# Kernel tuning notes

Hardware: AMD Instinct MI355X
Metric: run time of the kernel (lower is better)

The kernel has to match this reference:

```python
import jax, jax.numpy as jnp
import numpy as np

B, L, D, H = 4, 1024, 1024, 16
HD = D // H  # 64
MAX_LEN = 1024


def setup_inputs() -> dict:
    key = jax.random.key(0)
    k1, k2, k3, k4 = jax.random.split(key, 4)
    x = jax.random.normal(k1, (B, L, D), dtype=jnp.float32)
    W_qkv = jax.random.normal(k2, (D, 3 * D), dtype=jnp.float32) * (1.0 / np.sqrt(D))
    W_proj = jax.random.normal(k3, (D, D), dtype=jnp.float32) * (1.0 / np.sqrt(D))
    b_proj = jnp.zeros((D,), dtype=jnp.float32)
    rel_pos_emb = jax.random.normal(k4, (2 * MAX_LEN - 1, HD), dtype=jnp.float32)
    return {"x": x, "W_qkv": W_qkv, "W_proj": W_proj, "b_proj": b_proj,
            "rel_pos_emb": rel_pos_emb}


def reference(x, W_qkv, W_proj, b_proj, rel_pos_emb):
    b, l, d = x.shape
    scale = 1.0 / np.sqrt(HD)
    # fused qkv projection: [B, L, 3, H, HD]
    qkv = (x @ W_qkv).reshape(b, l, 3, H, HD)
    q = jnp.transpose(qkv[:, :, 0], (0, 2, 1, 3))  # [B, H, L, HD]
    k = jnp.transpose(qkv[:, :, 1], (0, 2, 1, 3))
    v = jnp.transpose(qkv[:, :, 2], (0, 2, 1, 3))
    # content scores
    attn = jnp.einsum('bhld,bhmd->bhlm', q, k) * scale
    # relative position scores: pos_indices[i, j] = (j - i) + (L - 1)
    pos_indices = (jnp.arange(l)[None, :] - jnp.arange(l)[:, None]) + (l - 1)
    rel_pos = rel_pos_emb[pos_indices]  # [L, L, HD]
    pos_attn = jnp.einsum('bhld,lkd->bhlk', q, rel_pos) * scale
    attn = jax.nn.softmax(attn + pos_attn, axis=-1)
    out = jnp.einsum('bhlm,bhmd->bhld', attn, v)  # [B, H, L, HD]
    out = jnp.transpose(out, (0, 2, 1, 3)).reshape(b, l, d)
    return out @ W_proj + b_proj
```

## Files before the change

kernel.cpp:

```cpp
#include <hip/hip_runtime.h>
#include <cstdint>

#define L_SEQ 1024
#define NH 16
#define HD 64
#define DMODEL 1024
#define BHS (L_SEQ * HD)

typedef __bf16 bf16x8 __attribute__((ext_vector_type(8)));
typedef float f32x4 __attribute__((ext_vector_type(4)));
typedef unsigned short u16x8 __attribute__((ext_vector_type(8)));

#define MFMA16(a, b, c) __builtin_amdgcn_mfma_f32_16x16x32_bf16((a), (b), (c), 0, 0, 0)

static __device__ __forceinline__ unsigned short f2b(float f) {
  unsigned int u = __builtin_bit_cast(unsigned int, f);
  u = (u + 0x7FFFu + ((u >> 16) & 1u)) >> 16;
  return (unsigned short)u;
}

static __device__ __forceinline__ bf16x8 ld8(const unsigned short* p) {
  return *(const bf16x8*)(p);
}

static __device__ __forceinline__ float bperm(int byteaddr, float v) {
  return __builtin_bit_cast(float,
      __builtin_amdgcn_ds_bpermute(byteaddr, __builtin_bit_cast(int, v)));
}

static __device__ __forceinline__ void gl_lds(const unsigned short* g,
                                              unsigned short* l) {
  auto gp = (const __attribute__((address_space(1))) unsigned int*)((uintptr_t)g);
  auto lp = (__attribute__((address_space(3))) unsigned int*)((uintptr_t)l);
  __builtin_amdgcn_global_load_lds(gp, lp, 16, 0, 0);
}

__global__ __launch_bounds__(256) void k_prep(
    const float* __restrict__ x,      unsigned short* __restrict__ xb,
    const float* __restrict__ relemb, unsigned short* __restrict__ eb,
    const float* __restrict__ Wqkv,   unsigned short* __restrict__ wtq,
    const float* __restrict__ Wproj,  unsigned short* __restrict__ wtp) {
  const int b = blockIdx.x, tid = threadIdx.x;
  if (b < 4224) {
    const float* src; unsigned short* dst; int i;
    if (b < 4096) { src = x; dst = xb; i = b * 256 + tid; }
    else          { src = relemb; dst = eb; i = (b - 4096) * 256 + tid; }
    const int n4 = (b < 4096) ? 1048576 : 32752;
    if (i < n4) {
      float4 v = *(const float4*)(src + (size_t)i * 4);
      ushort4 o;
      o.x = f2b(v.x); o.y = f2b(v.y); o.z = f2b(v.z); o.w = f2b(v.w);
      *(ushort4*)(dst + (size_t)i * 4) = o;
    }
  } else {
    __shared__ float tile[32][33];
    const float* src; unsigned short* dst; int bx, by, C;
    if (b < 7296) { src = Wqkv; dst = wtq; C = 3072; bx = (b - 4224) % 96; by = (b - 4224) / 96; }
    else          { src = Wproj; dst = wtp; C = 1024; bx = (b - 7296) % 32; by = (b - 7296) / 32; }
    const int R = 1024;
    const int c0 = bx * 32, r0 = by * 32;
    const int tx = tid & 31, ty = tid >> 5;
#pragma unroll
    for (int i = 0; i < 4; ++i)
      tile[ty + i * 8][tx] = src[(size_t)(r0 + ty + i * 8) * C + c0 + tx];
    __syncthreads();
#pragma unroll
    for (int i = 0; i < 4; ++i)
      dst[(size_t)(c0 + ty + i * 8) * R + r0 + tx] = f2b(tile[tx][ty + i * 8]);
  }
}

__global__ __launch_bounds__(256) void k_gemm_qkv(
    const unsigned short* __restrict__ xb,
    const unsigned short* __restrict__ wt,
    unsigned short* __restrict__ qw,
    unsigned short* __restrict__ kw,
    unsigned short* __restrict__ vtw) {
  __shared__ unsigned short As[128 * 64];
  __shared__ unsigned short Bs[128 * 64];
  const int tid = threadIdx.x;
  const int w = tid >> 6, lane = tid & 63;
  const int wm = w >> 1, wn = w & 1;
  const int lo = lane & 15, hi = lane >> 4;
  const int m0 = blockIdx.y * 128, n0 = blockIdx.x * 128;
  const int srow = lane >> 3, scol = lane & 7;

  f32x4 acc[4][4];
#pragma unroll
  for (int i = 0; i < 4; ++i)
#pragma unroll
    for (int j = 0; j < 4; ++j) acc[i][j] = (f32x4){0.f, 0.f, 0.f, 0.f};

  for (int kt = 0; kt < 16; ++kt) {
    const int k0 = kt * 64;
#pragma unroll
    for (int i = 0; i < 4; ++i) {
      const int slot = w * 4 + i;
      const int r = slot * 8 + srow;
      const int cs = (scol ^ (r & 7)) * 8;
      gl_lds(xb + (size_t)(m0 + r) * 1024 + k0 + cs, &As[slot * 512]);
      gl_lds(wt + (size_t)(n0 + r) * 1024 + k0 + cs, &Bs[slot * 512]);
    }
    __syncthreads();
    bf16x8 af[2][4], bg[2][4];
#pragma unroll
    for (int kk = 0; kk < 2; ++kk)
#pragma unroll
      for (int i = 0; i < 4; ++i) {
        const int ra = wm * 64 + i * 16 + lo;
        const int rb = wn * 64 + i * 16 + lo;
        af[kk][i] = ld8(&As[ra * 64 + (((kk * 4 + hi) ^ (lo & 7)) * 8)]);
        bg[kk][i] = ld8(&Bs[rb * 64 + (((kk * 4 + hi) ^ (lo & 7)) * 8)]);
      }
#pragma unroll
    for (int kk = 0; kk < 2; ++kk)
#pragma unroll
      for (int mf = 0; mf < 4; ++mf)
#pragma unroll
        for (int nf = 0; nf < 4; ++nf)
          acc[mf][nf] = MFMA16(af[kk][mf], bg[kk][nf], acc[mf][nf]);
    __syncthreads();
  }

  const int which = n0 >> 10;
#pragma unroll
  for (int mf = 0; mf < 4; ++mf) {
#pragma unroll
    for (int rr = 0; rr < 4; ++rr) {
      const int row = m0 + wm * 64 + mf * 16 + hi * 4 + rr;
      const int bb = row >> 10, ll = row & 1023;
#pragma unroll
      for (int nf = 0; nf < 4; ++nf) {
        const int col = n0 + wn * 64 + nf * 16 + lo;
        const int hc = col & 1023;
        const int hh = hc >> 6, dd = hc & 63;
        const unsigned short val = f2b(acc[mf][nf][rr]);
        const size_t bh = (size_t)(bb * NH + hh);
        if (which == 0)      qw[bh * BHS + ll * HD + dd] = val;
        else if (which == 1) kw[bh * BHS + ll * HD + dd] = val;
        else                 vtw[bh * BHS + dd * L_SEQ + ll] = val;
      }
    }
  }
}

__global__ __launch_bounds__(256, 2) void k_attn(
    const unsigned short* __restrict__ qw,
    const unsigned short* __restrict__ kw,
    const unsigned short* __restrict__ vtw,
    const unsigned short* __restrict__ ew,
    unsigned short* __restrict__ ow) {
  __shared__ unsigned short Kb[2][4096];
  __shared__ unsigned short Vb[2][4096];
  __shared__ unsigned short Ps[4][2][16][72];
  const int tid = threadIdx.x;
  const int w = tid >> 6, lane = tid & 63;
  const int lo = lane & 15, hi = lane >> 4;
  const int cw = lo & 7;
  const int lbid = (blockIdx.x & 7) * 64 + (blockIdx.x >> 3);
  const int bh = lbid >> 3, qb = lbid & 7;
  const int q0 = qb * 128;
  const int l0w = q0 + w * 32;
  const int bb = bh >> 4, hh = bh & 15;

  bf16x8 aQ[2][2];
#pragma unroll
  for (int s = 0; s < 2; ++s) {
    const unsigned short* qbase = qw + (size_t)bh * BHS + (l0w + s * 16 + lo) * HD;
    aQ[s][0] = ld8(qbase + hi * 8);
    aQ[s][1] = ld8(qbase + 32 + hi * 8);
  }

  const unsigned short* kbase = kw + (size_t)bh * BHS;
  const unsigned short* vbase = vtw + (size_t)bh * BHS;

  const u16x8 one_u = {0x3F80, 0x3F80, 0x3F80, 0x3F80,
                       0x3F80, 0x3F80, 0x3F80, 0x3F80};
  const bf16x8 onesf = __builtin_bit_cast(bf16x8, one_u);

  int gaddr[4];
  bool gpred[4];
#pragma unroll
  for (int r = 0; r < 4; ++r) {
    const int rho = hi * 4 + r;
    const int t = lo + 15 - rho;
    gaddr[r] = (hi * 16 + (t & 15)) * 4;
    gpred[r] = t >= 16;
  }

  auto stage = [&](int nxt, int tt) {
    const unsigned short* kt = kbase + (size_t)(tt * 64) * 64;
    const unsigned short* vt = vbase + tt * 64;
#pragma unroll
    for (int i = 0; i < 2; ++i) {
      const int n = (w * 2 + i) * 64 + lane;
      const int r = n >> 3, c = n & 7;
      gl_lds(kt + r * 64 + ((c ^ (r & 7)) * 8), &Kb[nxt][(w * 2 + i) * 512]);
    }
#pragma unroll
    for (int i = 0; i < 2; ++i) {
      const int n = (w * 2 + i) * 64 + lane;
      const int r = n >> 3, c = n & 7;
      gl_lds(vt + (size_t)r * 1024 + ((c ^ (r & 7)) * 8), &Vb[nxt][(w * 2 + i) * 512]);
    }
  };

  f32x4 acc_o[2][4];
  f32x4 acc_l[2];
#pragma unroll
  for (int s = 0; s < 2; ++s) {
    acc_l[s] = (f32x4){0.f, 0.f, 0.f, 0.f};
#pragma unroll
    for (int d = 0; d < 4; ++d) acc_o[s][d] = (f32x4){0.f, 0.f, 0.f, 0.f};
  }

  stage(0, 0);
  __syncthreads();

  for (int t = 0; t < 16; ++t) {
    const int cur = t & 1;

    const int xb = t * 64 - l0w + 992;
    bf16x8 ef[6][2];
#pragma unroll
    for (int f = 0; f < 6; ++f) {
      int er = xb + f * 16 + lo;
      er = er > 2046 ? 2046 : er;
      const unsigned short* erow = ew + (size_t)er * HD + hi * 8;
      ef[f][0] = ld8(erow);
      ef[f][1] = ld8(erow + 32);
    }

    if (t < 15) stage(cur ^ 1, t + 1);

    bf16x8 kf[4][2];
#pragma unroll
    for (int nf = 0; nf < 4; ++nf) {
      const unsigned short* kr = &Kb[cur][(nf * 16 + lo) * 64];
      kf[nf][0] = ld8(kr + ((hi ^ cw) * 8));
      kf[nf][1] = ld8(kr + (((4 + hi) ^ cw) * 8));
    }

    f32x4 acc_s[2][4];
    __builtin_amdgcn_s_setprio(1);
#pragma unroll
    for (int s = 0; s < 2; ++s)
#pragma unroll
      for (int nf = 0; nf < 4; ++nf) {
        f32x4 c = (f32x4){0.f, 0.f, 0.f, 0.f};
        c = MFMA16(aQ[s][0], kf[nf][0], c);
        c = MFMA16(aQ[s][1], kf[nf][1], c);
        acc_s[s][nf] = c;
      }
    __builtin_amdgcn_s_setprio(0);

    f32x4 G[2][5];
#pragma unroll
    for (int s = 0; s < 2; ++s) {
      const int fb = 1 - s;
#pragma unroll
      for (int gf = 0; gf < 5; ++gf) {
        f32x4 g = (f32x4){0.f, 0.f, 0.f, 0.f};
        g = MFMA16(aQ[s][0], ef[gf + fb][0], g);
        g = MFMA16(aQ[s][1], ef[gf + fb][1], g);
        G[s][gf] = g;
      }
    }
#pragma unroll
    for (int s = 0; s < 2; ++s)
#pragma unroll
      for (int gf = 0; gf < 5; ++gf)
#pragma unroll
        for (int r = 0; r < 4; ++r)
          G[s][gf][r] = bperm(gaddr[r], G[s][gf][r]);

#pragma unroll
    for (int s = 0; s < 2; ++s)
#pragma unroll
      for (int nf = 0; nf < 4; ++nf)
#pragma unroll
        for (int r = 0; r < 4; ++r) {
          const float g = gpred[r] ? G[s][nf + 1][r] : G[s][nf][r];
          Ps[w][s][hi * 4 + r][nf * 16 + lo] =
              f2b(__expf((acc_s[s][nf][r] + g) * 0.125f));
        }

    bf16x8 aP[2][2];
#pragma unroll
    for (int s = 0; s < 2; ++s) {
      aP[s][0] = ld8(&Ps[w][s][lo][hi * 8]);
      aP[s][1] = ld8(&Ps[w][s][lo][32 + hi * 8]);
    }

#pragma unroll
    for (int s = 0; s < 2; ++s) {
      acc_l[s] = MFMA16(aP[s][0], onesf, acc_l[s]);
      acc_l[s] = MFMA16(aP[s][1], onesf, acc_l[s]);
    }

    bf16x8 vf[4][2];
#pragma unroll
    for (int df = 0; df < 4; ++df) {
      const unsigned short* vr = &Vb[cur][(df * 16 + lo) * 64];
      vf[df][0] = ld8(vr + ((hi ^ cw) * 8));
      vf[df][1] = ld8(vr + (((4 + hi) ^ cw) * 8));
    }
    __builtin_amdgcn_s_setprio(1);
#pragma unroll
    for (int s = 0; s < 2; ++s)
#pragma unroll
      for (int df = 0; df < 4; ++df) {
        acc_o[s][df] = MFMA16(aP[s][0], vf[df][0], acc_o[s][df]);
        acc_o[s][df] = MFMA16(aP[s][1], vf[df][1], acc_o[s][df]);
      }
    __builtin_amdgcn_s_setprio(0);

    __syncthreads();
  }

#pragma unroll
  for (int s = 0; s < 2; ++s)
#pragma unroll
    for (int r = 0; r < 4; ++r) {
      const int l = l0w + s * 16 + hi * 4 + r;
      const float inv = 1.f / acc_l[s][r];
      unsigned short* orow = ow + ((size_t)(bb * L_SEQ + l)) * DMODEL + hh * HD;
#pragma unroll
      for (int df = 0; df < 4; ++df)
        orow[df * 16 + lo] = f2b(acc_o[s][df][r] * inv);
    }
}

__global__ __launch_bounds__(256) void k_gemm_proj(
    const unsigned short* __restrict__ ob,
    const unsigned short* __restrict__ wt,
    const float* __restrict__ bias,
    float* __restrict__ out) {
  __shared__ unsigned short As[128 * 64];
  __shared__ unsigned short Bs[128 * 64];
  const int tid = threadIdx.x;
  const int w = tid >> 6, lane = tid & 63;
  const int wm = w >> 1, wn = w & 1;
  const int lo = lane & 15, hi = lane >> 4;
  const int m0 = blockIdx.y * 128, n0 = blockIdx.x * 128;
  const int srow = lane >> 3, scol = lane & 7;

  f32x4 acc[4][4];
#pragma unroll
  for (int i = 0; i < 4; ++i)
#pragma unroll
    for (int j = 0; j < 4; ++j) acc[i][j] = (f32x4){0.f, 0.f, 0.f, 0.f};

  for (int kt = 0; kt < 16; ++kt) {
    const int k0 = kt * 64;
#pragma unroll
    for (int i = 0; i < 4; ++i) {
      const int slot = w * 4 + i;
      const int r = slot * 8 + srow;
      const int cs = (scol ^ (r & 7)) * 8;
      gl_lds(ob + (size_t)(m0 + r) * 1024 + k0 + cs, &As[slot * 512]);
      gl_lds(wt + (size_t)(n0 + r) * 1024 + k0 + cs, &Bs[slot * 512]);
    }
    __syncthreads();
    bf16x8 af[2][4], bg[2][4];
#pragma unroll
    for (int kk = 0; kk < 2; ++kk)
#pragma unroll
      for (int i = 0; i < 4; ++i) {
        const int ra = wm * 64 + i * 16 + lo;
        const int rb = wn * 64 + i * 16 + lo;
        af[kk][i] = ld8(&As[ra * 64 + (((kk * 4 + hi) ^ (lo & 7)) * 8)]);
        bg[kk][i] = ld8(&Bs[rb * 64 + (((kk * 4 + hi) ^ (lo & 7)) * 8)]);
      }
#pragma unroll
    for (int kk = 0; kk < 2; ++kk)
#pragma unroll
      for (int mf = 0; mf < 4; ++mf)
#pragma unroll
        for (int nf = 0; nf < 4; ++nf)
          acc[mf][nf] = MFMA16(af[kk][mf], bg[kk][nf], acc[mf][nf]);
    __syncthreads();
  }

#pragma unroll
  for (int mf = 0; mf < 4; ++mf) {
#pragma unroll
    for (int rr = 0; rr < 4; ++rr) {
      const int row = m0 + wm * 64 + mf * 16 + hi * 4 + rr;
#pragma unroll
      for (int nf = 0; nf < 4; ++nf) {
        const int col = n0 + wn * 64 + nf * 16 + lo;
        out[(size_t)row * 1024 + col] = acc[mf][nf][rr] + bias[col];
      }
    }
  }
}

extern "C" void kernel_launch(void* const* d_in, const int* in_sizes, int n_in,
                              void* d_out, int out_size, void* d_ws, size_t ws_size,
                              hipStream_t stream) {
  const float* x      = (const float*)d_in[0];
  const float* Wqkv   = (const float*)d_in[1];
  const float* Wproj  = (const float*)d_in[2];
  const float* bproj  = (const float*)d_in[3];
  const float* relemb = (const float*)d_in[4];
  float* out = (float*)d_out;

  char* ws = (char*)d_ws;
  size_t off = 0;
  auto alloc = [&](size_t bytes) -> unsigned short* {
    unsigned short* p = (unsigned short*)(ws + off);
    off += (bytes + 255) & ~(size_t)255;
    return p;
  };
  unsigned short* xb  = alloc((size_t)4096 * 1024 * 2);
  unsigned short* wtq = alloc((size_t)3072 * 1024 * 2);
  unsigned short* wtp = alloc((size_t)1024 * 1024 * 2);
  unsigned short* eb  = alloc((size_t)2047 * 64 * 2);
  unsigned short* qw_ = alloc((size_t)64 * BHS * 2);
  unsigned short* kw_ = alloc((size_t)64 * BHS * 2);
  unsigned short* vtw = alloc((size_t)64 * BHS * 2);
  unsigned short* ow  = alloc((size_t)4096 * 1024 * 2);

  k_prep<<<8320, 256, 0, stream>>>(x, xb, relemb, eb, Wqkv, wtq, Wproj, wtp);
  k_gemm_qkv<<<dim3(24, 32), 256, 0, stream>>>(xb, wtq, qw_, kw_, vtw);
  k_attn<<<512, 256, 0, stream>>>(qw_, kw_, vtw, eb, ow);
  k_gemm_proj<<<dim3(8, 32), 256, 0, stream>>>(ow, wtp, bproj, out);
}
```

Before: 126.7 us.

## Stage QKV epilogue through LDS and prefetch rel-pos rows one tile ahead

The QKV GEMM epilogue now writes bf16 results into shared memory (reusing the A/B tile buffers), transposing V tiles there, and then issues 16-byte coalesced global stores instead of scattered 2-byte stores. The attention loop double-buffers the relative-position embedding fragments in registers, loading tile t+1's rows while tile t is computed, with the loop manually unrolled by two to swap the buffers. This aims to cut uncoalesced write traffic and hide global load latency for the embedding rows. The cost is extra VGPR pressure in the attention kernel, which runs with 2-block occupancy, and an extra barrier in the GEMM epilogue.

```diff
diff --git a/kernel.cpp b/kernel.cpp
--- a/kernel.cpp
+++ b/kernel.cpp
@@ -76,8 +76,10 @@
     unsigned short* __restrict__ qw,
     unsigned short* __restrict__ kw,
     unsigned short* __restrict__ vtw) {
-  __shared__ unsigned short As[128 * 64];
-  __shared__ unsigned short Bs[128 * 64];
+  __shared__ unsigned short SAB[2 * 128 * 64];
+  unsigned short* As = SAB;
+  unsigned short* Bs = SAB + 128 * 64;
+  unsigned short* Cs = SAB;
   const int tid = threadIdx.x;
   const int w = tid >> 6, lane = tid & 63;
   const int wm = w >> 1, wn = w & 1;
@@ -123,23 +125,44 @@
   }
 
   const int which = n0 >> 10;
-#pragma unroll
-  for (int mf = 0; mf < 4; ++mf) {
-#pragma unroll
-    for (int rr = 0; rr < 4; ++rr) {
-      const int row = m0 + wm * 64 + mf * 16 + hi * 4 + rr;
-      const int bb = row >> 10, ll = row & 1023;
-#pragma unroll
-      for (int nf = 0; nf < 4; ++nf) {
-        const int col = n0 + wn * 64 + nf * 16 + lo;
-        const int hc = col & 1023;
-        const int hh = hc >> 6, dd = hc & 63;
-        const unsigned short val = f2b(acc[mf][nf][rr]);
-        const size_t bh = (size_t)(bb * NH + hh);
-        if (which == 0)      qw[bh * BHS + ll * HD + dd] = val;
-        else if (which == 1) kw[bh * BHS + ll * HD + dd] = val;
-        else                 vtw[bh * BHS + dd * L_SEQ + ll] = val;
-      }
+  if (which == 2) {
+#pragma unroll
+    for (int mf = 0; mf < 4; ++mf)
+#pragma unroll
+      for (int rr = 0; rr < 4; ++rr)
+#pragma unroll
+        for (int nf = 0; nf < 4; ++nf)
+          Cs[(wn * 64 + nf * 16 + lo) * 128 + (wm * 64 + mf * 16 + hi * 4 + rr)] =
+              f2b(acc[mf][nf][rr]);
+  } else {
+#pragma unroll
+    for (int mf = 0; mf < 4; ++mf)
+#pragma unroll
+      for (int rr = 0; rr < 4; ++rr)
+#pragma unroll
+        for (int nf = 0; nf < 4; ++nf)
+          Cs[(wm * 64 + mf * 16 + hi * 4 + rr) * 128 + (wn * 64 + nf * 16 + lo)] =
+              f2b(acc[mf][nf][rr]);
+  }
+  __syncthreads();
+#pragma unroll
+  for (int i = 0; i < 8; ++i) {
+    const int c = tid * 8 + i;
+    const int rl = c >> 4, co = (c & 15) * 8;
+    uint4 v = *(const uint4*)(&Cs[rl * 128 + co]);
+    if (which == 2) {
+      const int col = n0 + rl;
+      const int hc = col & 1023, hh = hc >> 6, dd = hc & 63;
+      const int row = m0 + co;
+      const int bb2 = row >> 10, ll = row & 1023;
+      *(uint4*)(vtw + (size_t)(bb2 * NH + hh) * BHS + dd * L_SEQ + ll) = v;
+    } else {
+      const int row = m0 + rl;
+      const int bb2 = row >> 10, ll = row & 1023;
+      const int col = n0 + co;
+      const int hc = col & 1023, hh = hc >> 6, dd = hc & 63;
+      unsigned short* dst = (which == 0 ? qw : kw);
+      *(uint4*)(dst + (size_t)(bb2 * NH + hh) * BHS + ll * HD + dd) = v;
     }
   }
 }
@@ -205,33 +228,36 @@
     }
   };
 
-  f32x4 acc_o[2][4];
-  f32x4 acc_l[2];
-#pragma unroll
-  for (int s = 0; s < 2; ++s) {
-    acc_l[s] = (f32x4){0.f, 0.f, 0.f, 0.f};
-#pragma unroll
-    for (int d = 0; d < 4; ++d) acc_o[s][d] = (f32x4){0.f, 0.f, 0.f, 0.f};
-  }
-
-  stage(0, 0);
-  __syncthreads();
-
-  for (int t = 0; t < 16; ++t) {
-    const int cur = t & 1;
-
-    const int xb = t * 64 - l0w + 992;
-    bf16x8 ef[6][2];
+  auto loadE = [&](bf16x8 (&dst)[6][2], int tt) {
+    const int xb = tt * 64 - l0w + 992;
 #pragma unroll
     for (int f = 0; f < 6; ++f) {
       int er = xb + f * 16 + lo;
       er = er > 2046 ? 2046 : er;
       const unsigned short* erow = ew + (size_t)er * HD + hi * 8;
-      ef[f][0] = ld8(erow);
-      ef[f][1] = ld8(erow + 32);
-    }
-
-    if (t < 15) stage(cur ^ 1, t + 1);
+      dst[f][0] = ld8(erow);
+      dst[f][1] = ld8(erow + 32);
+    }
+  };
+
+  f32x4 acc_o[2][4];
+  f32x4 acc_l[2];
+#pragma unroll
+  for (int s = 0; s < 2; ++s) {
+    acc_l[s] = (f32x4){0.f, 0.f, 0.f, 0.f};
+#pragma unroll
+    for (int d = 0; d < 4; ++d) acc_o[s][d] = (f32x4){0.f, 0.f, 0.f, 0.f};
+  }
+
+  bf16x8 efA[6][2], efB[6][2];
+  loadE(efA, 0);
+  stage(0, 0);
+  __syncthreads();
+
+  auto body = [&](int t, int cur, bf16x8 (&efC)[6][2], bf16x8 (&efN)[6][2],
+                  bool doNext) {
+    if (doNext) loadE(efN, t + 1);
+    if (doNext) stage(cur ^ 1, t + 1);
 
     bf16x8 kf[4][2];
 #pragma unroll
@@ -261,8 +287,8 @@
 #pragma unroll
       for (int gf = 0; gf < 5; ++gf) {
         f32x4 g = (f32x4){0.f, 0.f, 0.f, 0.f};
-        g = MFMA16(aQ[s][0], ef[gf + fb][0], g);
-        g = MFMA16(aQ[s][1], ef[gf + fb][1], g);
+        g = MFMA16(aQ[s][0], efC[gf + fb][0], g);
+        g = MFMA16(aQ[s][1], efC[gf + fb][1], g);
         G[s][gf] = g;
       }
     }
@@ -316,6 +342,12 @@
     __builtin_amdgcn_s_setprio(0);
 
     __syncthreads();
+  };
+
+#pragma unroll 1
+  for (int tp = 0; tp < 8; ++tp) {
+    body(2 * tp,     0, efA, efB, true);
+    body(2 * tp + 1, 1, efB, efA, tp < 7);
   }
 
 #pragma unroll
```

Result: slower. 179.1 us (+41.4%).

## Stage 128-key K/V tiles and process two sub-passes per barrier

Applied to the files above, without the earlier changes.

The attention loop now stages K and V in 128-key tiles and processes each tile in two 64-key sub-passes, so each block goes through 8 barriers instead of 16. The prefetch of the next tile is issued between the two sub-passes. The P scratch buffer is shrunk to one slot per wave and reused across the two query sub-tiles. V fragments are loaded before the softmax writes. LDS use per block grows, which may limit occupancy and changes how much prefetch overlaps with compute.

```diff
diff --git a/kernel.cpp b/kernel.cpp
--- a/kernel.cpp
+++ b/kernel.cpp
@@ -150,9 +150,9 @@
     const unsigned short* __restrict__ vtw,
     const unsigned short* __restrict__ ew,
     unsigned short* __restrict__ ow) {
-  __shared__ unsigned short Kb[2][4096];
-  __shared__ unsigned short Vb[2][4096];
-  __shared__ unsigned short Ps[4][2][16][72];
+  __shared__ unsigned short Kb[2][8192];
+  __shared__ unsigned short Vb[2][8192];
+  __shared__ unsigned short Ps[4][16][72];
   const int tid = threadIdx.x;
   const int w = tid >> 6, lane = tid & 63;
   const int lo = lane & 15, hi = lane >> 4;
@@ -188,20 +188,22 @@
     gpred[r] = t >= 16;
   }
 
-  auto stage = [&](int nxt, int tt) {
-    const unsigned short* kt = kbase + (size_t)(tt * 64) * 64;
-    const unsigned short* vt = vbase + tt * 64;
-#pragma unroll
-    for (int i = 0; i < 2; ++i) {
-      const int n = (w * 2 + i) * 64 + lane;
+  auto stage = [&](int nxt, int it2) {
+    const unsigned short* kt = kbase + (size_t)it2 * 128 * 64;
+    const unsigned short* vt = vbase + it2 * 128;
+#pragma unroll
+    for (int i = 0; i < 4; ++i) {
+      const int n = (w * 4 + i) * 64 + lane;
       const int r = n >> 3, c = n & 7;
-      gl_lds(kt + r * 64 + ((c ^ (r & 7)) * 8), &Kb[nxt][(w * 2 + i) * 512]);
-    }
-#pragma unroll
-    for (int i = 0; i < 2; ++i) {
-      const int n = (w * 2 + i) * 64 + lane;
-      const int r = n >> 3, c = n & 7;
-      gl_lds(vt + (size_t)r * 1024 + ((c ^ (r & 7)) * 8), &Vb[nxt][(w * 2 + i) * 512]);
+      gl_lds(kt + r * 64 + ((c ^ (r & 7)) * 8), &Kb[nxt][(w * 4 + i) * 512]);
+    }
+#pragma unroll
+    for (int i = 0; i < 4; ++i) {
+      const int n = (w * 4 + i) * 64 + lane;
+      const int m = n >> 3, c = n & 7;
+      const int hhalf = m >> 6, dd = m & 63;
+      gl_lds(vt + (size_t)dd * 1024 + hhalf * 64 + ((c ^ (m & 7)) * 8),
+             &Vb[nxt][(w * 4 + i) * 512]);
     }
   };
 
@@ -217,26 +219,22 @@
   stage(0, 0);
   __syncthreads();
 
-  for (int t = 0; t < 16; ++t) {
-    const int cur = t & 1;
-
-    const int xb = t * 64 - l0w + 992;
+  auto pass = [&](int cur, int p, int tAbs) {
+    const int xbase = tAbs * 64 - l0w + 992;
     bf16x8 ef[6][2];
 #pragma unroll
     for (int f = 0; f < 6; ++f) {
-      int er = xb + f * 16 + lo;
+      int er = xbase + f * 16 + lo;
       er = er > 2046 ? 2046 : er;
       const unsigned short* erow = ew + (size_t)er * HD + hi * 8;
       ef[f][0] = ld8(erow);
       ef[f][1] = ld8(erow + 32);
     }
 
-    if (t < 15) stage(cur ^ 1, t + 1);
-
     bf16x8 kf[4][2];
 #pragma unroll
     for (int nf = 0; nf < 4; ++nf) {
-      const unsigned short* kr = &Kb[cur][(nf * 16 + lo) * 64];
+      const unsigned short* kr = &Kb[cur][(p * 64 + nf * 16 + lo) * 64];
       kf[nf][0] = ld8(kr + ((hi ^ cw) * 8));
       kf[nf][1] = ld8(kr + (((4 + hi) ^ cw) * 8));
     }
@@ -274,47 +272,44 @@
         for (int r = 0; r < 4; ++r)
           G[s][gf][r] = bperm(gaddr[r], G[s][gf][r]);
 
-#pragma unroll
-    for (int s = 0; s < 2; ++s)
+    bf16x8 vf[4][2];
+#pragma unroll
+    for (int df = 0; df < 4; ++df) {
+      const unsigned short* vr = &Vb[cur][(p * 64 + df * 16 + lo) * 64];
+      vf[df][0] = ld8(vr + ((hi ^ cw) * 8));
+      vf[df][1] = ld8(vr + (((4 + hi) ^ cw) * 8));
+    }
+
+#pragma unroll
+    for (int s = 0; s < 2; ++s) {
 #pragma unroll
       for (int nf = 0; nf < 4; ++nf)
 #pragma unroll
         for (int r = 0; r < 4; ++r) {
           const float g = gpred[r] ? G[s][nf + 1][r] : G[s][nf][r];
-          Ps[w][s][hi * 4 + r][nf * 16 + lo] =
+          Ps[w][hi * 4 + r][nf * 16 + lo] =
               f2b(__expf((acc_s[s][nf][r] + g) * 0.125f));
         }
-
-    bf16x8 aP[2][2];
-#pragma unroll
-    for (int s = 0; s < 2; ++s) {
-      aP[s][0] = ld8(&Ps[w][s][lo][hi * 8]);
-      aP[s][1] = ld8(&Ps[w][s][lo][32 + hi * 8]);
-    }
-
-#pragma unroll
-    for (int s = 0; s < 2; ++s) {
-      acc_l[s] = MFMA16(aP[s][0], onesf, acc_l[s]);
-      acc_l[s] = MFMA16(aP[s][1], onesf, acc_l[s]);
-    }
-
-    bf16x8 vf[4][2];
-#pragma unroll
-    for (int df = 0; df < 4; ++df) {
-      const unsigned short* vr = &Vb[cur][(df * 16 + lo) * 64];
-      vf[df][0] = ld8(vr + ((hi ^ cw) * 8));
-      vf[df][1] = ld8(vr + (((4 + hi) ^ cw) * 8));
-    }
-    __builtin_amdgcn_s_setprio(1);
-#pragma unroll
-    for (int s = 0; s < 2; ++s)
+      const bf16x8 aP0 = ld8(&Ps[w][lo][hi * 8]);
+      const bf16x8 aP1 = ld8(&Ps[w][lo][32 + hi * 8]);
+      acc_l[s] = MFMA16(aP0, onesf, acc_l[s]);
+      acc_l[s] = MFMA16(aP1, onesf, acc_l[s]);
+      __builtin_amdgcn_s_setprio(1);
 #pragma unroll
       for (int df = 0; df < 4; ++df) {
-        acc_o[s][df] = MFMA16(aP[s][0], vf[df][0], acc_o[s][df]);
-        acc_o[s][df] = MFMA16(aP[s][1], vf[df][1], acc_o[s][df]);
-      }
-    __builtin_amdgcn_s_setprio(0);
-
+        acc_o[s][df] = MFMA16(aP0, vf[df][0], acc_o[s][df]);
+        acc_o[s][df] = MFMA16(aP1, vf[df][1], acc_o[s][df]);
+      }
+      __builtin_amdgcn_s_setprio(0);
+    }
+  };
+
+#pragma unroll 1
+  for (int it = 0; it < 8; ++it) {
+    const int cur = it & 1;
+    pass(cur, 0, 2 * it);
+    if (it < 7) stage(cur ^ 1, it + 1);
+    pass(cur, 1, 2 * it + 1);
     __syncthreads();
   }
 
```

Measured after the change: 124.6 us. About the same (-1.6%).
